# Kernel optimization log

Measured on AMD Instinct MI355X. Metric: run time of the kernel, lower is better.

## Reference

```python
import jax, jax.numpy as jnp
import numpy as np

HEAD_SIZE = 64

def setup_inputs() -> dict:
    key = jax.random.key(0)
    k1, k2, k3, k4 = jax.random.split(key, 4)
    B, T, C = 4, 4096, 768
    s = 1.0 / np.sqrt(C)
    return {
        "x": jax.random.normal(k1, (B, T, C), dtype=jnp.float32),
        "Wq": jax.random.normal(k2, (C, HEAD_SIZE), dtype=jnp.float32) * s,
        "Wk": jax.random.normal(k3, (C, HEAD_SIZE), dtype=jnp.float32) * s,
        "Wv": jax.random.normal(k4, (C, HEAD_SIZE), dtype=jnp.float32) * s,
    }

def reference(x, Wq, Wk, Wv):
    # x: [B,T,C]; Wq/Wk/Wv: [C,H]
    T = x.shape[1]
    q = jnp.einsum('btc,ch->bth', x, Wq)
    k = jnp.einsum('btc,ch->bth', x, Wk)
    v = jnp.einsum('btc,ch->bth', x, Wv)
    scale = HEAD_SIZE ** (-0.5)
    wei = jnp.einsum('bth,bsh->bts', q, k) * scale  # [B,T,T]
    causal = jnp.tril(jnp.ones((T, T), dtype=bool))
    wei = jnp.where(causal, wei, -jnp.inf)
    wei = jax.nn.softmax(wei, axis=-1)
    # dropout p=0.0 -> identity
    out = jnp.einsum('bts,bsh->bth', wei, v)  # [B,T,H]
    return out
```

## Files before the change

kernel.cpp:

```cpp
#include <hip/hip_runtime.h>
#include <hip/hip_bf16.h>
#include <stdint.h>

typedef unsigned short u16;
typedef __attribute__((ext_vector_type(8))) __bf16 bf16x8;
typedef __attribute__((ext_vector_type(4))) float f32x4;

#define LOG2E 1.44269504088896340736f
#define FIXED_M 16.0f

__device__ inline u16 f2bf(float f){
  uint32_t u = __float_as_uint(f);
  u += 0x7FFFu + ((u >> 16) & 1u);
  return (u16)(u >> 16);
}
__device__ inline float bf2f(u16 v){
  return __uint_as_float(((uint32_t)v) << 16);
}

__global__ __launch_bounds__(256) void wt_kernel(const float* __restrict__ Wq,
                                                 const float* __restrict__ Wk,
                                                 const float* __restrict__ Wv,
                                                 u16* __restrict__ wtf){
  int idx = blockIdx.x * 256 + threadIdx.x;
  if (idx >= 192 * 768) return;
  int n = idx / 768, c = idx - n * 768;
  int h = n & 63;
  const float* W = (n < 64) ? Wq : ((n < 128) ? Wk : Wv);
  float v = W[c * 64 + h];
  if (n < 64) v *= 0.125f * LOG2E;
  int f = n >> 4, n16 = n & 15;
  int kstep = c >> 5, quad = (c >> 3) & 3, j = c & 7;
  wtf[(size_t)((f * 24 + kstep) * 64 + quad * 16 + n16) * 8 + j] = f2bf(v);
}

__global__ __launch_bounds__(256) void proj_kernel(const float* __restrict__ x,
                                                   const u16* __restrict__ wtf,
                                                   u16* __restrict__ qs,
                                                   u16* __restrict__ ks,
                                                   u16* __restrict__ vt){
  __shared__ float red[4][16][196];
  const int tid = threadIdx.x;
  const int w = tid >> 6, lane = tid & 63;
  const int n16 = lane & 15, quad = lane >> 4;
  const int rt = blockIdx.x * 16;
  const float* xr = x + (size_t)(rt + n16) * 768 + w * 192;

  const f32x4 fz = {0.f, 0.f, 0.f, 0.f};
  f32x4 acc[12];
#pragma unroll
  for (int f = 0; f < 12; ++f) acc[f] = fz;

#pragma unroll
  for (int kl = 0; kl < 6; ++kl){
    const float4 xa = *(const float4*)(xr + kl * 32 + quad * 8);
    const float4 xb = *(const float4*)(xr + kl * 32 + quad * 8 + 4);
    union { bf16x8 v; u16 e[8]; } ua;
    ua.e[0] = f2bf(xa.x); ua.e[1] = f2bf(xa.y);
    ua.e[2] = f2bf(xa.z); ua.e[3] = f2bf(xa.w);
    ua.e[4] = f2bf(xb.x); ua.e[5] = f2bf(xb.y);
    ua.e[6] = f2bf(xb.z); ua.e[7] = f2bf(xb.w);
#pragma unroll
    for (int f = 0; f < 12; ++f){
      bf16x8 bfrag = *(const bf16x8*)(wtf + (size_t)((f * 24 + w * 6 + kl) * 64 + lane) * 8);
      acc[f] = __builtin_amdgcn_mfma_f32_16x16x32_bf16(ua.v, bfrag, acc[f], 0, 0, 0);
    }
  }

#pragma unroll
  for (int f = 0; f < 12; ++f){
#pragma unroll
    for (int r = 0; r < 4; ++r)
      red[w][quad * 4 + r][f * 16 + n16] = acc[f][r];
  }
  __syncthreads();

  const int m = tid & 15, cg = tid >> 4;
  const int orow = rt + m;
  const int b = orow >> 12, t = orow & 4095;
#pragma unroll
  for (int i = 0; i < 12; ++i){
    int n = cg * 12 + i;
    float s = red[0][m][n] + red[1][m][n] + red[2][m][n] + red[3][m][n];
    u16 val = f2bf(s);
    if (n < 64)       qs[(size_t)orow * 64 + n]        = val;
    else if (n < 128) ks[(size_t)orow * 64 + (n - 64)] = val;
    else              vt[((size_t)b * 64 + (n - 128)) * 4096 + t] = val;
  }
}

__global__ __launch_bounds__(256) void flash_part(const u16* __restrict__ qs,
                                                  const u16* __restrict__ ks,
                                                  const u16* __restrict__ vtg,
                                                  u16* __restrict__ Opart,
                                                  float* __restrict__ ml){
  const int b  = blockIdx.x >> 9;
  const int qt = (blockIdx.x >> 3) & 63;
  const int ck = blockIdx.x & 7;
  const int kt0 = ck * 8;
  if (kt0 > qt) return;
  const int kt1 = min(qt, kt0 + 7);

  __shared__ u16 Ks[64 * 72];
  __shared__ u16 Vt[64 * 72];
  __shared__ u16 Ps[4 * 16 * 72];
  const int tid = threadIdx.x;
  const int w = tid >> 6, lane = tid & 63;
  const int n16 = lane & 15, quad = lane >> 4;
  const size_t bo = (size_t)b * 4096 * 64;
  const u16* qb = qs + bo;
  const u16* kb = ks + bo;
  const u16* vb = vtg + bo;

  const int qrow = qt * 64 + w * 16 + n16;
  bf16x8 qA0 = *(const bf16x8*)(qb + (size_t)qrow * 64 + quad * 8);
  bf16x8 qA1 = *(const bf16x8*)(qb + (size_t)qrow * 64 + 32 + quad * 8);

  const f32x4 fz = {0.f, 0.f, 0.f, 0.f};
  f32x4 O[4];
  float rs[4] = {0.f, 0.f, 0.f, 0.f};
#pragma unroll
  for (int f = 0; f < 4; ++f) O[f] = fz;

  const int c0r = tid >> 3,          c0p = tid & 7;
  const int c1r = (tid + 256) >> 3,  c1p = tid & 7;

  uint4 rk0 = *(const uint4*)(kb + (size_t)kt0 * 4096 + c0r * 64 + c0p * 8);
  uint4 rk1 = *(const uint4*)(kb + (size_t)kt0 * 4096 + c1r * 64 + c1p * 8);
  uint4 rv0 = *(const uint4*)(vb + (size_t)c0r * 4096 + kt0 * 64 + c0p * 8);
  uint4 rv1 = *(const uint4*)(vb + (size_t)c1r * 4096 + kt0 * 64 + c1p * 8);

  for (int kt = kt0; kt <= kt1; ++kt){
    *(uint4*)&Ks[c0r * 72 + c0p * 8] = rk0;
    *(uint4*)&Ks[c1r * 72 + c1p * 8] = rk1;
    *(uint4*)&Vt[c0r * 72 + c0p * 8] = rv0;
    *(uint4*)&Vt[c1r * 72 + c1p * 8] = rv1;
    __syncthreads();

    if (kt < kt1){
      rk0 = *(const uint4*)(kb + (size_t)(kt + 1) * 4096 + c0r * 64 + c0p * 8);
      rk1 = *(const uint4*)(kb + (size_t)(kt + 1) * 4096 + c1r * 64 + c1p * 8);
      rv0 = *(const uint4*)(vb + (size_t)c0r * 4096 + (kt + 1) * 64 + c0p * 8);
      rv1 = *(const uint4*)(vb + (size_t)c1r * 4096 + (kt + 1) * 64 + c1p * 8);
    }

    f32x4 S[4];
#pragma unroll
    for (int f = 0; f < 4; ++f){
      bf16x8 b0 = *(const bf16x8*)&Ks[(f * 16 + n16) * 72 + quad * 8];
      bf16x8 b1 = *(const bf16x8*)&Ks[(f * 16 + n16) * 72 + 32 + quad * 8];
      f32x4 s = fz;
      s = __builtin_amdgcn_mfma_f32_16x16x32_bf16(qA0, b0, s, 0, 0, 0);
      s = __builtin_amdgcn_mfma_f32_16x16x32_bf16(qA1, b1, s, 0, 0, 0);
      S[f] = s;
    }

    if (kt == qt){
#pragma unroll
      for (int f = 0; f < 4; ++f){
#pragma unroll
        for (int r = 0; r < 4; ++r){
          int col = kt * 64 + f * 16 + n16;
          int row = qt * 64 + w * 16 + quad * 4 + r;
          if (col > row) S[f][r] = -1e30f;
        }
      }
    }

#pragma unroll
    for (int f = 0; f < 4; ++f){
#pragma unroll
      for (int r = 0; r < 4; ++r){
        float p = __builtin_amdgcn_exp2f(S[f][r] - FIXED_M);
        S[f][r] = p;
        rs[r] += p;
      }
    }

#pragma unroll
    for (int f = 0; f < 4; ++f){
#pragma unroll
      for (int r = 0; r < 4; ++r)
        Ps[(w * 16 + quad * 4 + r) * 72 + f * 16 + n16] = f2bf(S[f][r]);
    }
    bf16x8 pA0 = *(const bf16x8*)&Ps[(w * 16 + n16) * 72 + quad * 8];
    bf16x8 pA1 = *(const bf16x8*)&Ps[(w * 16 + n16) * 72 + 32 + quad * 8];

#pragma unroll
    for (int f = 0; f < 4; ++f){
      bf16x8 v0 = *(const bf16x8*)&Vt[(f * 16 + n16) * 72 + quad * 8];
      bf16x8 v1 = *(const bf16x8*)&Vt[(f * 16 + n16) * 72 + 32 + quad * 8];
      O[f] = __builtin_amdgcn_mfma_f32_16x16x32_bf16(pA0, v0, O[f], 0, 0, 0);
      O[f] = __builtin_amdgcn_mfma_f32_16x16x32_bf16(pA1, v1, O[f], 0, 0, 0);
    }
    __syncthreads();
  }

#pragma unroll
  for (int r = 0; r < 4; ++r){
#pragma unroll
    for (int off = 1; off < 16; off <<= 1)
      rs[r] += __shfl_xor(rs[r], off, 16);
  }

  const size_t oidx = (size_t)blockIdx.x * 4096;
#pragma unroll
  for (int f = 0; f < 4; ++f){
#pragma unroll
    for (int r = 0; r < 4; ++r){
      int row_local = w * 16 + quad * 4 + r;
      Opart[oidx + (size_t)row_local * 64 + f * 16 + n16] = f2bf(O[f][r]);
    }
  }
  if (n16 == 0){
    float* lp = ml + (size_t)blockIdx.x * 64;
#pragma unroll
    for (int r = 0; r < 4; ++r)
      lp[w * 16 + quad * 4 + r] = rs[r];
  }
}

__global__ __launch_bounds__(256) void combine_kernel(const u16* __restrict__ Opart,
                                                      const float* __restrict__ ml,
                                                      float* __restrict__ out){
  const int gid = blockIdx.x * 256 + threadIdx.x;
  const size_t base = (size_t)gid * 4;
  const int bq = gid >> 10;
  const int rem = (int)(base & 4095);
  const int row = rem >> 6;
  const int qt = bq & 63;
  const int nc = (qt >> 3) + 1;

  float L = 0.f;
  float a0 = 0.f, a1 = 0.f, a2 = 0.f, a3 = 0.f;
  for (int c = 0; c < nc; ++c){
    L += ml[((size_t)bq * 8 + c) * 64 + row];
    const u16* p = Opart + ((size_t)bq * 8 + c) * 4096 + rem;
    uint2 d = *(const uint2*)p;
    a0 += bf2f((u16)(d.x & 0xffffu));
    a1 += bf2f((u16)(d.x >> 16));
    a2 += bf2f((u16)(d.y & 0xffffu));
    a3 += bf2f((u16)(d.y >> 16));
  }
  const float invL = 1.0f / L;
  float4 v = {a0 * invL, a1 * invL, a2 * invL, a3 * invL};
  *(float4*)(out + base) = v;
}

extern "C" void kernel_launch(void* const* d_in, const int* in_sizes, int n_in,
                              void* d_out, int out_size, void* d_ws, size_t ws_size,
                              hipStream_t stream){
  const float* x  = (const float*)d_in[0];
  const float* Wq = (const float*)d_in[1];
  const float* Wk = (const float*)d_in[2];
  const float* Wv = (const float*)d_in[3];
  float* out = (float*)d_out;

  u16* qs = (u16*)d_ws;
  u16* ks = qs + (size_t)16384 * 64;
  u16* vt = ks + (size_t)16384 * 64;
  u16* wtf = vt + (size_t)16384 * 64;
  u16* Opart = wtf + (size_t)192 * 768;
  float* ml = (float*)(Opart + (size_t)2048 * 4096);

  wt_kernel<<<576, 256, 0, stream>>>(Wq, Wk, Wv, wtf);
  proj_kernel<<<1024, 256, 0, stream>>>(x, wtf, qs, ks, vt);
  flash_part<<<2048, 256, 0, stream>>>(qs, ks, vt, Opart, ml);
  combine_kernel<<<1024, 256, 0, stream>>>(Opart, ml, out);
}
```

Baseline: 148.5 us.

## Restructure projection: stage bf16 x tile in swizzled LDS, split output columns per wave

The projection kernel now processes 32 rows per block. It loads the x tile with coalesced float4 reads, converts it to bf16 and stores it in a swizzled LDS layout. Each wave then computes a distinct slice of output columns over the full K=768, instead of splitting K across waves and reducing partial sums through shared memory. This removes the fp32 LDS reduction and the extra sync, and reuses each weight fragment across two row groups. The trade-offs are fewer blocks (512), a long serial K loop per wave, and less latency hiding while the tile is staged.

```diff
diff --git a/kernel.cpp b/kernel.cpp
--- a/kernel.cpp
+++ b/kernel.cpp
@@ -37,55 +37,73 @@
 __global__ __launch_bounds__(256) void proj_kernel(const float* __restrict__ x,
                                                    const u16* __restrict__ wtf,
                                                    u16* __restrict__ qs,
-                                                   u16* __restrict__ ks,
+                                                   u16* __restrict__ kso,
                                                    u16* __restrict__ vt){
-  __shared__ float red[4][16][196];
+  __shared__ u16 At[2 * 24 * 64 * 8];
   const int tid = threadIdx.x;
   const int w = tid >> 6, lane = tid & 63;
   const int n16 = lane & 15, quad = lane >> 4;
-  const int rt = blockIdx.x * 16;
-  const float* xr = x + (size_t)(rt + n16) * 768 + w * 192;
+  const int rt = blockIdx.x * 32;
+
+  const float* xb = x + (size_t)rt * 768;
+  for (int p = 0; p < 3; ++p){
+    float4 t[8];
+#pragma unroll
+    for (int i = 0; i < 8; ++i)
+      t[i] = *(const float4*)(xb + (size_t)((p * 8 + i) * 256 + tid) * 4);
+#pragma unroll
+    for (int i = 0; i < 8; ++i){
+      int l = (p * 8 + i) * 256 + tid;
+      int row = l / 192, c4 = l - row * 192;
+      int g = row >> 4, r16 = row & 15;
+      int ksn = c4 >> 3, qd = (c4 >> 1) & 3, j0 = (c4 & 1) * 4;
+      int idx = (((g * 24 + ksn) * 64 + qd * 16 + r16) * 8 + j0) ^ ((ksn & 7) << 3);
+      union { ushort4 s; u16 e[4]; } pk;
+      pk.e[0] = f2bf(t[i].x); pk.e[1] = f2bf(t[i].y);
+      pk.e[2] = f2bf(t[i].z); pk.e[3] = f2bf(t[i].w);
+      *(ushort4*)&At[idx] = pk.s;
+    }
+  }
+  __syncthreads();
 
   const f32x4 fz = {0.f, 0.f, 0.f, 0.f};
-  f32x4 acc[12];
-#pragma unroll
-  for (int f = 0; f < 12; ++f) acc[f] = fz;
-
-#pragma unroll
-  for (int kl = 0; kl < 6; ++kl){
-    const float4 xa = *(const float4*)(xr + kl * 32 + quad * 8);
-    const float4 xb = *(const float4*)(xr + kl * 32 + quad * 8 + 4);
-    union { bf16x8 v; u16 e[8]; } ua;
-    ua.e[0] = f2bf(xa.x); ua.e[1] = f2bf(xa.y);
-    ua.e[2] = f2bf(xa.z); ua.e[3] = f2bf(xa.w);
-    ua.e[4] = f2bf(xb.x); ua.e[5] = f2bf(xb.y);
-    ua.e[6] = f2bf(xb.z); ua.e[7] = f2bf(xb.w);
-#pragma unroll
-    for (int f = 0; f < 12; ++f){
-      bf16x8 bfrag = *(const bf16x8*)(wtf + (size_t)((f * 24 + w * 6 + kl) * 64 + lane) * 8);
-      acc[f] = __builtin_amdgcn_mfma_f32_16x16x32_bf16(ua.v, bfrag, acc[f], 0, 0, 0);
-    }
-  }
-
-#pragma unroll
-  for (int f = 0; f < 12; ++f){
-#pragma unroll
-    for (int r = 0; r < 4; ++r)
-      red[w][quad * 4 + r][f * 16 + n16] = acc[f][r];
-  }
-  __syncthreads();
-
-  const int m = tid & 15, cg = tid >> 4;
-  const int orow = rt + m;
-  const int b = orow >> 12, t = orow & 4095;
-#pragma unroll
-  for (int i = 0; i < 12; ++i){
-    int n = cg * 12 + i;
-    float s = red[0][m][n] + red[1][m][n] + red[2][m][n] + red[3][m][n];
-    u16 val = f2bf(s);
-    if (n < 64)       qs[(size_t)orow * 64 + n]        = val;
-    else if (n < 128) ks[(size_t)orow * 64 + (n - 64)] = val;
-    else              vt[((size_t)b * 64 + (n - 128)) * 4096 + t] = val;
+  f32x4 acc[2][3];
+#pragma unroll
+  for (int g = 0; g < 2; ++g)
+#pragma unroll
+    for (int j = 0; j < 3; ++j) acc[g][j] = fz;
+
+#pragma unroll
+  for (int kst = 0; kst < 24; ++kst){
+    const int sw = (kst & 7) << 3;
+    bf16x8 a0 = *(const bf16x8*)&At[(((0 * 24 + kst) * 64 + lane) * 8) ^ sw];
+    bf16x8 a1 = *(const bf16x8*)&At[(((1 * 24 + kst) * 64 + lane) * 8) ^ sw];
+#pragma unroll
+    for (int j = 0; j < 3; ++j){
+      bf16x8 bfr = *(const bf16x8*)(wtf + (size_t)(((3 * w + j) * 24 + kst) * 64 + lane) * 8);
+      acc[0][j] = __builtin_amdgcn_mfma_f32_16x16x32_bf16(a0, bfr, acc[0][j], 0, 0, 0);
+      acc[1][j] = __builtin_amdgcn_mfma_f32_16x16x32_bf16(a1, bfr, acc[1][j], 0, 0, 0);
+    }
+  }
+
+  const int bb = rt >> 12, t0 = rt & 4095;
+#pragma unroll
+  for (int j = 0; j < 3; ++j){
+    const int F = 3 * w + j;
+#pragma unroll
+    for (int g = 0; g < 2; ++g){
+#pragma unroll
+      for (int r = 0; r < 4; ++r){
+        u16 val = f2bf(acc[g][j][r]);
+        int row = rt + g * 16 + quad * 4 + r;
+        if (F < 4)
+          qs[(size_t)row * 64 + F * 16 + n16] = val;
+        else if (F < 8)
+          kso[(size_t)row * 64 + (F - 4) * 16 + n16] = val;
+        else
+          vt[((size_t)bb * 64 + (F - 8) * 16 + n16) * 4096 + t0 + g * 16 + quad * 4 + r] = val;
+      }
+    }
   }
 }
 
@@ -264,7 +282,7 @@
   float* ml = (float*)(Opart + (size_t)2048 * 4096);
 
   wt_kernel<<<576, 256, 0, stream>>>(Wq, Wk, Wv, wtf);
-  proj_kernel<<<1024, 256, 0, stream>>>(x, wtf, qs, ks, vt);
+  proj_kernel<<<512, 256, 0, stream>>>(x, wtf, qs, ks, vt);
   flash_part<<<2048, 256, 0, stream>>>(qs, ks, vt, Opart, ml);
   combine_kernel<<<1024, 256, 0, stream>>>(Opart, ml, out);
 }
```

After: 141.2 us. 1.05x faster.
